# Kernel optimization log

Measured on AMD Instinct MI355X. Metric: run time of the kernel, lower is better.

The kernel has to match this reference:

```python
import jax, jax.numpy as jnp
import numpy as np

B, S, E, H = 1, 2048, 1024, 16
D = E // H  # head_dim = 64
MAX_POS = 2048
NEG_INF = -1e30


def _rotary(x):
    # x: [B, S, H, D]; positions along axis 1
    half = D // 2
    inv_freq = 1.0 / (10000.0 ** (jnp.arange(0, D, 2, dtype=jnp.float32) / D))  # [D/2]
    freqs = jnp.arange(S, dtype=jnp.float32)[:, None] * inv_freq[None, :]       # [S, D/2]
    emb = jnp.concatenate([freqs, freqs], axis=-1)                              # [S, D]
    cos = jnp.cos(emb)[None, :, None, :]
    sin = jnp.sin(emb)[None, :, None, :]
    x1, x2 = x[..., :half], x[..., half:]
    rot = jnp.concatenate([-x2, x1], axis=-1)
    return x * cos + rot * sin


def setup_inputs() -> dict:
    key = jax.random.key(0)
    ks = jax.random.split(key, 8)
    w = lambda k: (jax.random.normal(k, (E, E), jnp.float32) * 0.02)
    inp = {
        "x": jax.random.normal(ks[0], (B, S, E), jnp.float32),
        "mask": jnp.tril(jnp.ones((S, S), jnp.int32)),  # causal 0/1 mask
        "Wq": w(ks[1]), "bq": jnp.zeros((E,), jnp.float32),
        "Wk": w(ks[2]), "bk": jnp.zeros((E,), jnp.float32),
        "Wv": w(ks[3]), "bv": jnp.zeros((E,), jnp.float32),
        "Wo": w(ks[4]), "bo": jnp.zeros((E,), jnp.float32),
        "rel_pos_emb": jax.random.normal(ks[5], (2 * MAX_POS - 1, D), jnp.float32) * 0.02,
    }
    return inp


def reference(x, mask, Wq, bq, Wk, bk, Wv, bv, Wo, bo, rel_pos_emb):
    scale = D ** -0.5
    q = (x @ Wq + bq).reshape(B, S, H, D)
    k = (x @ Wk + bk).reshape(B, S, H, D)
    v = (x @ Wv + bv).reshape(B, S, H, D)
    q = _rotary(q)
    k = _rotary(k)
    # [B, H, S, D]
    qh = jnp.swapaxes(q, 1, 2)
    kh = jnp.swapaxes(k, 1, 2)
    vh = jnp.swapaxes(v, 1, 2)
    scores = jnp.einsum('bhid,bhjd->bhij', qh, kh) * scale  # [B,H,S,S]
    # relative position bias (Shaw-style: gather then contract with q)
    pos = jnp.arange(S)
    bucket = pos[None, :] - pos[:, None] + S - 1            # [S,S] in [0, 2S-2]
    rel = rel_pos_emb[bucket]                               # [S,S,D]
    scores = scores + jnp.einsum('bhid,ijd->bhij', qh, rel)
    scores = jnp.where(mask[None, None, :, :] == 0, NEG_INF, scores)
    attn = jax.nn.softmax(scores, axis=-1)
    out = jnp.einsum('bhij,bhjd->bhid', attn, vh)           # [B,H,S,D]
    out = jnp.swapaxes(out, 1, 2).reshape(B, S, E)
    return out @ Wo + bo
```

## Files before the change

### kernel.cpp

```cpp
#include <hip/hip_runtime.h>
#include <hip/hip_bf16.h>

typedef __attribute__((ext_vector_type(8))) short bf16x8;
typedef __attribute__((ext_vector_type(4))) float f32x4;

#define MFMA16(a,b,c) __builtin_amdgcn_mfma_f32_16x16x32_bf16((a),(b),(c),0,0,0)
#define GLDS16(g, l) __builtin_amdgcn_global_load_lds((const __attribute__((address_space(1))) void*)(g), (__attribute__((address_space(3))) void*)(l), 16, 0, 0)

static constexpr int S_ = 2048, E_ = 1024, H_ = 16;
static constexpr float QS = 0.125f * 1.44269504f;

__device__ __forceinline__ unsigned pk2(float a, float b) {
  __hip_bfloat16 ba = __float2bfloat16(a), bb = __float2bfloat16(b);
  return (unsigned)*(unsigned short*)&ba | ((unsigned)*(unsigned short*)&bb << 16);
}
__device__ __forceinline__ float ubf(unsigned short u) {
  return __uint_as_float((unsigned)u << 16);
}

__global__ __launch_bounds__(256) void prep_k(const float* __restrict__ x, const float* __restrict__ rel,
                                              const float* __restrict__ Wq, const float* __restrict__ Wk,
                                              const float* __restrict__ Wv, const float* __restrict__ Wo,
                                              const float* __restrict__ bq, const float* __restrict__ bk,
                                              const float* __restrict__ bv,
                                              __hip_bfloat16* __restrict__ xb, __hip_bfloat16* __restrict__ relb,
                                              __hip_bfloat16* __restrict__ wqkvT, __hip_bfloat16* __restrict__ woT,
                                              float* __restrict__ bqkv, float* __restrict__ cost,
                                              float* __restrict__ sint) {
  int blk = blockIdx.x, tid = threadIdx.x;
  if (blk < 1024) {
    __shared__ float tile[64][65];
    int wsel = blk >> 8, sub = blk & 255;
    const float* W = wsel == 0 ? Wq : wsel == 1 ? Wk : wsel == 2 ? Wv : Wo;
    __hip_bfloat16* WT = wsel < 3 ? wqkvT + (size_t)wsel * E_ * E_ : woT;
    int bx = sub & 15, by = sub >> 4;
    for (int i = tid; i < 4096; i += 256) {
      int ki = i >> 6, ni = i & 63;
      tile[ki][ni] = W[(size_t)(by*64 + ki) * E_ + bx*64 + ni];
    }
    __syncthreads();
    for (int i = tid; i < 4096; i += 256) {
      int ni = i >> 6, ki = i & 63;
      WT[(size_t)(bx*64 + ni) * E_ + by*64 + ki] = __float2bfloat16(tile[ki][ni]);
    }
  } else if (blk < 3072) {
    int i = (blk - 1024) * 256 + tid;
    float4 v = reinterpret_cast<const float4*>(x)[i];
    xb[4*i+0] = __float2bfloat16(v.x);
    xb[4*i+1] = __float2bfloat16(v.y);
    xb[4*i+2] = __float2bfloat16(v.z);
    xb[4*i+3] = __float2bfloat16(v.w);
  } else if (blk < 3328) {
    int i = (blk - 3072) * 256 + tid;
    if (i < 65520) {
      float4 v = reinterpret_cast<const float4*>(rel)[i];
      relb[4*i+0] = __float2bfloat16(v.x * 8.f);
      relb[4*i+1] = __float2bfloat16(v.y * 8.f);
      relb[4*i+2] = __float2bfloat16(v.z * 8.f);
      relb[4*i+3] = __float2bfloat16(v.w * 8.f);
    }
  } else if (blk < 3584) {
    int idx = (blk - 3328) * 256 + tid;
    int f = idx & 31, s = idx >> 5;
    float inv = powf(10000.f, -(float)f * (1.f/32.f));
    float a = (float)s * inv;
    cost[idx] = cosf(a);
    sint[idx] = sinf(a);
  } else {
    int i = (blk - 3584) * 256 + tid;
    if (i < 3072) bqkv[i] = i < 1024 ? bq[i] : (i < 2048 ? bk[i-1024] : bv[i-2048]);
  }
}

template<int BM, int MODE>
__global__ __launch_bounds__(256) void gemm_k(const __hip_bfloat16* __restrict__ A,
                                              const __hip_bfloat16* __restrict__ BT,
                                              const float* __restrict__ bias,
                                              const float* __restrict__ cost,
                                              const float* __restrict__ sint,
                                              __hip_bfloat16* __restrict__ qhh,
                                              __hip_bfloat16* __restrict__ khh,
                                              __hip_bfloat16* __restrict__ vt,
                                              float* __restrict__ outf,
                                              int K) {
  constexpr int MI = BM/32;
  __shared__ __hip_bfloat16 As[2][BM*64];
  __shared__ __hip_bfloat16 Bs[2][128*64];
  int tid = threadIdx.x, lane = tid & 63, w = tid >> 6;
  int rowq = lane & 15, hi = lane >> 4, ksel = hi << 3;
  int wr = (w >> 1) * (BM/2), wc = (w & 1) * 64;
  int m0 = blockIdx.y * BM, n0 = blockIdx.x * 128;
  int l3 = lane >> 3, l7 = lane & 7;
  f32x4 acc[MI][4] = {};

  auto stage = [&](int k0, int buf) {
    const char* Ap = (const char*)A + ((size_t)(m0 + w*(BM/4)) * K + k0) * 2;
    const char* Bp = (const char*)BT + ((size_t)(n0 + w*32) * K + k0) * 2;
    char* Ad = (char*)&As[buf][w*(BM/4)*64];
    char* Bd = (char*)&Bs[buf][w*32*64];
    for (int i = 0; i < MI; ++i)
      GLDS16(Ap + (size_t)(i*8 + l3)*(K*2) + l7*16, Ad + i*1024);
    for (int i = 0; i < 4; ++i)
      GLDS16(Bp + (size_t)(i*8 + l3)*(K*2) + l7*16, Bd + i*1024);
  };

  stage(0, 0);
  __syncthreads();
  int buf = 0;
  int nk = K >> 6;
  for (int t = 0; t < nk; ++t) {
    if (t + 1 < nk) stage((t+1)*64, buf^1);
    for (int kk = 0; kk < 64; kk += 32) {
      bf16x8 a[MI], b[4];
      for (int i = 0; i < MI; ++i) a[i] = *(const bf16x8*)&As[buf][(wr + i*16 + rowq)*64 + kk + ksel];
      for (int j = 0; j < 4; ++j)  b[j] = *(const bf16x8*)&Bs[buf][(wc + j*16 + rowq)*64 + kk + ksel];
      for (int i = 0; i < MI; ++i)
        for (int j = 0; j < 4; ++j)
          acc[i][j] = MFMA16(a[i], b[j], acc[i][j]);
    }
    __syncthreads();
    buf ^= 1;
  }

  if constexpr (MODE == 0) {
    int matsel = n0 >> 10, ncol = n0 & 1023;
    float bcol[4];
    for (int j = 0; j < 4; ++j) bcol[j] = bias[n0 + wc + j*16 + rowq];
    if (matsel < 2) {
      __hip_bfloat16* dst = matsel ? khh : qhh;
      float qs = matsel ? 1.0f : QS;
      for (int i = 0; i < MI; ++i)
        for (int rg = 0; rg < 4; ++rg) {
          int s = m0 + wr + i*16 + hi*4 + rg;
          for (int j = 0; j < 2; ++j) {
            int colp = ncol + wc + j*16 + rowq;
            int hh = colp >> 6, f = colp & 31;
            float c = cost[s*32 + f], sn = sint[s*32 + f];
            float v1 = acc[i][j][rg]   + bcol[j];
            float v2 = acc[i][j+2][rg] + bcol[j+2];
            dst[((size_t)hh*S_ + s)*64 + f]      = __float2bfloat16((v1*c - v2*sn) * qs);
            dst[((size_t)hh*S_ + s)*64 + f + 32] = __float2bfloat16((v2*c + v1*sn) * qs);
          }
        }
    } else {
      for (int i = 0; i < MI; ++i)
        for (int j = 0; j < 4; ++j) {
          int colp = ncol + wc + j*16 + rowq;
          int hh = colp >> 6, d = colp & 63;
          int s0b = m0 + wr + i*16 + hi*4;
          __hip_bfloat16 tmp[4];
          for (int rg = 0; rg < 4; ++rg)
            tmp[rg] = __float2bfloat16(acc[i][j][rg] + bcol[j]);
          *(ushort4*)(vt + ((size_t)hh*64 + d)*S_ + s0b) = *(ushort4*)tmp;
        }
    }
  } else {
    for (int i = 0; i < MI; ++i)
      for (int rg = 0; rg < 4; ++rg) {
        int row = m0 + wr + i*16 + hi*4 + rg;
        for (int j = 0; j < 4; ++j) {
          int col = n0 + wc + j*16 + rowq;
          outf[(size_t)row*E_ + col] = acc[i][j][rg] + bias[col];
        }
      }
  }
}

__global__ __launch_bounds__(256,2) void attn_k(const __hip_bfloat16* __restrict__ qh,
                                                const __hip_bfloat16* __restrict__ kh,
                                                const __hip_bfloat16* __restrict__ vt,
                                                const __hip_bfloat16* __restrict__ relb,
                                                __hip_bfloat16* __restrict__ opart,
                                                float2* __restrict__ ml) {
  int h = blockIdx.x & 15, p = blockIdx.x >> 4;
  int tid = threadIdx.x, lane = tid & 63, w = tid >> 6;
  int rowq = lane & 15, hi = lane >> 4, ksel = hi << 3;
  int l3 = lane >> 3, l7 = lane & 7;
  int swz = (l7*16) ^ (l3 << 4);
  __shared__ __hip_bfloat16 Ks[2][4096];
  __shared__ __hip_bfloat16 Vs[2][4096];
  __shared__ float Wf[4][16*82];
  __shared__ char  Psb[4][4096];
  float* wrow = &Wf[w][rowq*82];
  char* pp = Psb[w] + rowq*256;
  int sw8 = (rowq & 7) << 4;
  int pcol0 = ((hi*16)      ^ ((rowq & 7) << 4)) >> 1;
  int pcol1 = ((64 + hi*16) ^ ((rowq & 7) << 4)) >> 1;
  int c0 = hi*4 + 15 - rowq;

  for (int ph = 0; ph < 2; ++ph) {
    int qb = ph ? 31 - p : p;
    int T = qb + 1;
    int t0 = ph ? (T + 1) >> 1 : 0;
    int t1 = ph ? T : (T + 1) >> 1;
    int i0w = qb*64 + w*16;

    const __hip_bfloat16* qrow = qh + ((size_t)h*S_ + i0w + rowq)*64 + ksel;
    bf16x8 q0 = *(const bf16x8*)(qrow);
    bf16x8 q1 = *(const bf16x8*)(qrow + 32);
    f32x4 o[4] = {};
    float m = -1e30f, l = 0.f;

    auto stage = [&](int t, int buf) {
      int j0 = t * 64;
      const char* kp = (const char*)(kh + ((size_t)h*S_ + j0 + w*16)*64);
      const char* vp = (const char*)(vt + ((size_t)(h*64 + w*16))*S_ + j0);
      char* kd = (char*)&Ks[buf][w*16*64];
      char* vd = (char*)&Vs[buf][w*16*64];
      for (int i = 0; i < 2; ++i) {
        GLDS16(kp + (size_t)(i*8 + l3)*128  + swz, kd + i*1024);
        GLDS16(vp + (size_t)(i*8 + l3)*4096 + swz, vd + i*1024);
      }
    };
    auto ldrel = [&](int t, bf16x8* rr) {
      const __hip_bfloat16* rp = relb + (size_t)(t*64 - i0w + 2032 + rowq)*64 + ksel;
      #pragma unroll
      for (int nf = 0; nf < 5; ++nf) {
        rr[nf*2]   = *(const bf16x8*)(rp + nf*1024);
        rr[nf*2+1] = *(const bf16x8*)(rp + nf*1024 + 32);
      }
    };

    if (t0 < t1) {
      bf16x8 rc[10];
      ldrel(t0, rc);
      stage(t0, 0);
      __syncthreads();
      int buf = 0;
      for (int t = t0; t < t1; ++t) {
        bool more = (t + 1 < t1);
        if (more) stage(t+1, buf^1);

        f32x4 sa[4] = {};
        f32x4 wt[5] = {};
        __builtin_amdgcn_s_setprio(1);
        for (int kk = 0; kk < 2; ++kk) {
          bf16x8 qf = kk ? q1 : q0;
          int pc = kk ? pcol1 : pcol0;
          for (int nf = 0; nf < 4; ++nf) {
            bf16x8 kf = *(const bf16x8*)&Ks[buf][(nf*16 + rowq)*64 + pc];
            sa[nf] = MFMA16(kf, qf, sa[nf]);
          }
          for (int nf = 0; nf < 5; ++nf)
            wt[nf] = MFMA16(rc[nf*2+kk], qf, wt[nf]);
        }
        __builtin_amdgcn_s_setprio(0);

        #pragma unroll
        for (int nf = 0; nf < 5; ++nf) {
          *(float2*)(wrow + nf*16 + hi*4)     = make_float2(wt[nf][0], wt[nf][1]);
          *(float2*)(wrow + nf*16 + hi*4 + 2) = make_float2(wt[nf][2], wt[nf][3]);
        }

        if (more) ldrel(t+1, rc);

        float sv[4][4];
        #pragma unroll
        for (int rg = 0; rg < 4; ++rg) {
          int cc = c0 + rg;
          #pragma unroll
          for (int nf = 0; nf < 4; ++nf)
            sv[nf][rg] = sa[nf][rg] + wrow[nf*16 + cc];
        }
        float tm = -1e30f;
        bool diag = (t == qb);
        int lim = w*16 + rowq;
        #pragma unroll
        for (int nf = 0; nf < 4; ++nf)
          #pragma unroll
          for (int rg = 0; rg < 4; ++rg) {
            int kl = nf*16 + hi*4 + rg;
            if (diag && kl > lim) sv[nf][rg] = -1e30f;
            tm = fmaxf(tm, sv[nf][rg]);
          }
        tm = fmaxf(tm, __shfl_xor(tm, 16));
        tm = fmaxf(tm, __shfl_xor(tm, 32));

        bool defer = __all(tm <= m + 8.0f);
        float al = 1.0f;
        if (!defer) {
          float mnew = fmaxf(m, tm);
          al = exp2f(m - mnew);
          m = mnew;
        }
        float ls = 0.f;
        float pe[4][4];
        #pragma unroll
        for (int nf = 0; nf < 4; ++nf)
          #pragma unroll
          for (int rg = 0; rg < 4; ++rg) {
            float e = exp2f(sv[nf][rg] - m);
            pe[nf][rg] = e;
            ls += e;
          }
        l = l * al + ls;
        #pragma unroll
        for (int nf = 0; nf < 4; ++nf) {
          uint2 u = { pk2(pe[nf][0], pe[nf][1]), pk2(pe[nf][2], pe[nf][3]) };
          *(uint2*)(pp + ((nf*32 + hi*8) ^ sw8)) = u;
        }
        if (!defer) {
          float alq[4];
          #pragma unroll
          for (int rg = 0; rg < 4; ++rg) alq[rg] = __shfl(al, hi*4 + rg, 16);
          #pragma unroll
          for (int df = 0; df < 4; ++df)
            #pragma unroll
            for (int rg = 0; rg < 4; ++rg) o[df][rg] *= alq[rg];
        }

        __builtin_amdgcn_s_setprio(1);
        for (int kk = 0; kk < 2; ++kk) {
          bf16x8 a = *(const bf16x8*)(pp + ((kk*64 + hi*16) ^ sw8));
          int pc = kk ? pcol1 : pcol0;
          for (int df = 0; df < 4; ++df) {
            bf16x8 b = *(const bf16x8*)&Vs[buf][(df*16 + rowq)*64 + pc];
            o[df] = MFMA16(a, b, o[df]);
          }
        }
        __builtin_amdgcn_s_setprio(0);
        __syncthreads();
        buf ^= 1;
      }
    }

    float lt = l;
    lt += __shfl_xor(lt, 16);
    lt += __shfl_xor(lt, 32);
    if (lane < 16) ml[((size_t)ph*S_ + i0w + rowq)*H_ + h] = make_float2(m, lt);
    #pragma unroll
    for (int df = 0; df < 4; ++df)
      #pragma unroll
      for (int rg = 0; rg < 4; ++rg)
        opart[(size_t)ph*S_*E_ + (size_t)(i0w + hi*4 + rg)*E_ + h*64 + df*16 + rowq] =
            __float2bfloat16(o[df][rg]);
    __syncthreads();
  }
}

__global__ __launch_bounds__(256) void combine_k(const __hip_bfloat16* __restrict__ opart,
                                                 const float2* __restrict__ ml,
                                                 __hip_bfloat16* __restrict__ aout) {
  int r = blockIdx.x, tid = threadIdx.x;
  int c = tid * 4, h = c >> 6;
  float2 a0 = ml[(size_t)r*H_ + h];
  float2 a1 = ml[((size_t)S_ + r)*H_ + h];
  float M = fmaxf(a0.x, a1.x);
  float w0 = exp2f(a0.x - M), w1 = exp2f(a1.x - M);
  float dinv = 1.0f / (w0*a0.y + w1*a1.y);
  w0 *= dinv; w1 *= dinv;
  const unsigned short* o0 = (const unsigned short*)opart + (size_t)r*E_ + c;
  const unsigned short* o1 = o0 + (size_t)S_*E_;
  ushort4 u0 = *(const ushort4*)o0;
  ushort4 u1 = *(const ushort4*)o1;
  __hip_bfloat16 res[4];
  res[0] = __float2bfloat16(w0*ubf(u0.x) + w1*ubf(u1.x));
  res[1] = __float2bfloat16(w0*ubf(u0.y) + w1*ubf(u1.y));
  res[2] = __float2bfloat16(w0*ubf(u0.z) + w1*ubf(u1.z));
  res[3] = __float2bfloat16(w0*ubf(u0.w) + w1*ubf(u1.w));
  *(ushort4*)((unsigned short*)aout + (size_t)r*E_ + c) = *(ushort4*)res;
}

extern "C" void kernel_launch(void* const* d_in, const int* in_sizes, int n_in,
                              void* d_out, int out_size, void* d_ws, size_t ws_size,
                              hipStream_t stream) {
  const float* x   = (const float*)d_in[0];
  const float* Wq  = (const float*)d_in[2];
  const float* bq  = (const float*)d_in[3];
  const float* Wk  = (const float*)d_in[4];
  const float* bk  = (const float*)d_in[5];
  const float* Wv  = (const float*)d_in[6];
  const float* bv  = (const float*)d_in[7];
  const float* Wo  = (const float*)d_in[8];
  const float* bo  = (const float*)d_in[9];
  const float* rel = (const float*)d_in[10];
  float* out = (float*)d_out;

  char* ws = (char*)d_ws;
  size_t off = 0;
  auto alloc = [&](size_t bytes) -> void* {
    void* p = ws + off;
    off = (off + bytes + 255) & ~(size_t)255;
    return p;
  };
  __hip_bfloat16* xb    = (__hip_bfloat16*)alloc((size_t)S_*E_*2);
  __hip_bfloat16* wqkvT = (__hip_bfloat16*)alloc((size_t)3*E_*E_*2);
  float* cost = (float*)alloc((size_t)S_*32*4);
  float* sint = (float*)alloc((size_t)S_*32*4);
  float* bqkv = (float*)alloc((size_t)3072*4);
  if (off < (size_t)16*1024*1024) off = (size_t)16*1024*1024;
  __hip_bfloat16* woT   = (__hip_bfloat16*)alloc((size_t)E_*E_*2);
  __hip_bfloat16* relb  = (__hip_bfloat16*)alloc((size_t)4095*64*2);
  __hip_bfloat16* qhh  = (__hip_bfloat16*)alloc((size_t)S_*E_*2);
  __hip_bfloat16* khh  = (__hip_bfloat16*)alloc((size_t)S_*E_*2);
  __hip_bfloat16* vth  = (__hip_bfloat16*)alloc((size_t)S_*E_*2);
  __hip_bfloat16* aout = (__hip_bfloat16*)alloc((size_t)S_*E_*2);
  float2* ml = (float2*)alloc((size_t)2*S_*H_*8);

  __hip_bfloat16* opart = (__hip_bfloat16*)ws;

  prep_k<<<3596, 256, 0, stream>>>(x, rel, Wq, Wk, Wv, Wo, bq, bk, bv,
                                   xb, relb, wqkvT, woT, bqkv, cost, sint);

  gemm_k<64,0><<<dim3(24,32), 256, 0, stream>>>(xb, wqkvT, bqkv, cost, sint,
                                                qhh, khh, vth, nullptr, E_);

  attn_k<<<512, 256, 0, stream>>>(qhh, khh, vth, relb, opart, ml);
  combine_k<<<S_, 256, 0, stream>>>(opart, ml, aout);

  gemm_k<64,1><<<dim3(8,32), 256, 0, stream>>>(aout, woT, bo, nullptr, nullptr,
                                               nullptr, nullptr, nullptr, out, E_);
}
```

Baseline: 114.4 us.

## Software-pipeline QK and rel-bias MFMAs one tile ahead of softmax

Restructures the attention inner loop so the QK^T and relative-position MFMAs for tile t+1 are issued before the softmax and PV work of tile t. A prologue computes the first tile's scores. K and V loads are staged two tiles ahead, which needs a third V buffer in LDS. The goal is to overlap MFMA work with the softmax VALU and LDS latency. The cost is more registers for the extra score and bias accumulators and about 8KB more LDS per block, which could hurt occupancy.

```diff
diff --git a/kernel.cpp b/kernel.cpp
--- a/kernel.cpp
+++ b/kernel.cpp
@@ -178,7 +178,7 @@
   int l3 = lane >> 3, l7 = lane & 7;
   int swz = (l7*16) ^ (l3 << 4);
   __shared__ __hip_bfloat16 Ks[2][4096];
-  __shared__ __hip_bfloat16 Vs[2][4096];
+  __shared__ __hip_bfloat16 Vs[3][4096];
   __shared__ float Wf[4][16*82];
   __shared__ char  Psb[4][4096];
   float* wrow = &Wf[w][rowq*82];
@@ -201,12 +201,13 @@
     f32x4 o[4] = {};
     float m = -1e30f, l = 0.f;
 
-    auto stage = [&](int t, int buf) {
+    auto stage = [&](int t) {
       int j0 = t * 64;
+      int kb = t & 1, vbuf = t % 3;
       const char* kp = (const char*)(kh + ((size_t)h*S_ + j0 + w*16)*64);
       const char* vp = (const char*)(vt + ((size_t)(h*64 + w*16))*S_ + j0);
-      char* kd = (char*)&Ks[buf][w*16*64];
-      char* vd = (char*)&Vs[buf][w*16*64];
+      char* kd = (char*)&Ks[kb][w*16*64];
+      char* vd = (char*)&Vs[vbuf][w*16*64];
       for (int i = 0; i < 2; ++i) {
         GLDS16(kp + (size_t)(i*8 + l3)*128  + swz, kd + i*1024);
         GLDS16(vp + (size_t)(i*8 + l3)*4096 + swz, vd + i*1024);
@@ -220,39 +221,55 @@
         rr[nf*2+1] = *(const bf16x8*)(rp + nf*1024 + 32);
       }
     };
+    auto qkw = [&](int t, bf16x8* rr, f32x4* sa, f32x4* wt) {
+      int kb = t & 1;
+      __builtin_amdgcn_s_setprio(1);
+      #pragma unroll
+      for (int kk = 0; kk < 2; ++kk) {
+        bf16x8 qf = kk ? q1 : q0;
+        int pc = kk ? pcol1 : pcol0;
+        #pragma unroll
+        for (int nf = 0; nf < 4; ++nf) {
+          bf16x8 kf = *(const bf16x8*)&Ks[kb][(nf*16 + rowq)*64 + pc];
+          sa[nf] = MFMA16(kf, qf, sa[nf]);
+        }
+        #pragma unroll
+        for (int nf = 0; nf < 5; ++nf)
+          wt[nf] = MFMA16(rr[nf*2+kk], qf, wt[nf]);
+      }
+      __builtin_amdgcn_s_setprio(0);
+    };
+    auto wstore = [&](f32x4* wt) {
+      #pragma unroll
+      for (int nf = 0; nf < 5; ++nf) {
+        *(float2*)(wrow + nf*16 + hi*4)     = make_float2(wt[nf][0], wt[nf][1]);
+        *(float2*)(wrow + nf*16 + hi*4 + 2) = make_float2(wt[nf][2], wt[nf][3]);
+      }
+    };
 
     if (t0 < t1) {
       bf16x8 rc[10];
+      stage(t0);
       ldrel(t0, rc);
-      stage(t0, 0);
       __syncthreads();
-      int buf = 0;
+      if (t0 + 1 < t1) stage(t0 + 1);
+      f32x4 saP[4] = {};
+      {
+        f32x4 wtP[5] = {};
+        qkw(t0, rc, saP, wtP);
+        wstore(wtP);
+      }
+      if (t0 + 1 < t1) ldrel(t0 + 1, rc);
+      __syncthreads();
+
       for (int t = t0; t < t1; ++t) {
         bool more = (t + 1 < t1);
-        if (more) stage(t+1, buf^1);
-
-        f32x4 sa[4] = {};
-        f32x4 wt[5] = {};
-        __builtin_amdgcn_s_setprio(1);
-        for (int kk = 0; kk < 2; ++kk) {
-          bf16x8 qf = kk ? q1 : q0;
-          int pc = kk ? pcol1 : pcol0;
-          for (int nf = 0; nf < 4; ++nf) {
-            bf16x8 kf = *(const bf16x8*)&Ks[buf][(nf*16 + rowq)*64 + pc];
-            sa[nf] = MFMA16(kf, qf, sa[nf]);
-          }
-          for (int nf = 0; nf < 5; ++nf)
-            wt[nf] = MFMA16(rc[nf*2+kk], qf, wt[nf]);
-        }
-        __builtin_amdgcn_s_setprio(0);
-
-        #pragma unroll
-        for (int nf = 0; nf < 5; ++nf) {
-          *(float2*)(wrow + nf*16 + hi*4)     = make_float2(wt[nf][0], wt[nf][1]);
-          *(float2*)(wrow + nf*16 + hi*4 + 2) = make_float2(wt[nf][2], wt[nf][3]);
-        }
-
-        if (more) ldrel(t+1, rc);
+        if (t + 2 < t1) stage(t + 2);
+
+        f32x4 saN[4] = {};
+        f32x4 wtN[5] = {};
+        if (more) qkw(t + 1, rc, saN, wtN);
+        if (t + 2 < t1) ldrel(t + 2, rc);
 
         float sv[4][4];
         #pragma unroll
@@ -260,7 +277,7 @@
           int cc = c0 + rg;
           #pragma unroll
           for (int nf = 0; nf < 4; ++nf)
-            sv[nf][rg] = sa[nf][rg] + wrow[nf*16 + cc];
+            sv[nf][rg] = saP[nf][rg] + wrow[nf*16 + cc];
         }
         float tm = -1e30f;
         bool diag = (t == qb);
@@ -309,18 +326,26 @@
             for (int rg = 0; rg < 4; ++rg) o[df][rg] *= alq[rg];
         }
 
+        int vbuf = t % 3;
         __builtin_amdgcn_s_setprio(1);
+        #pragma unroll
         for (int kk = 0; kk < 2; ++kk) {
           bf16x8 a = *(const bf16x8*)(pp + ((kk*64 + hi*16) ^ sw8));
           int pc = kk ? pcol1 : pcol0;
+          #pragma unroll
           for (int df = 0; df < 4; ++df) {
-            bf16x8 b = *(const bf16x8*)&Vs[buf][(df*16 + rowq)*64 + pc];
+            bf16x8 b = *(const bf16x8*)&Vs[vbuf][(df*16 + rowq)*64 + pc];
             o[df] = MFMA16(a, b, o[df]);
           }
         }
         __builtin_amdgcn_s_setprio(0);
+
+        if (more) {
+          wstore(wtN);
+          #pragma unroll
+          for (int nf = 0; nf < 4; ++nf) saP[nf] = saN[nf];
+        }
         __syncthreads();
-        buf ^= 1;
       }
     }
 
```

New measurement: 118.2 us. +3.3%, slower.

## Fuse split-softmax combine into output projection GEMM A-tile staging

Applied to the files above, without the earlier changes.

Removes the separate combine kernel and its intermediate bf16 buffer. The output-projection GEMM gains a new mode that, while staging each A tile, reads both partial attention outputs plus their max and sum statistics, merges them and writes bf16 into shared memory. This saves one kernel launch and a full write and read of the merged activations. In exchange, the A-tile loads become synchronous register loads instead of async global-to-LDS copies, and each of the 8 column blocks recomputes the merge, so partial outputs are read several times.

```diff
diff --git a/kernel.cpp b/kernel.cpp
--- a/kernel.cpp
+++ b/kernel.cpp
@@ -82,6 +82,7 @@
                                               __hip_bfloat16* __restrict__ khh,
                                               __hip_bfloat16* __restrict__ vt,
                                               float* __restrict__ outf,
+                                              const float2* __restrict__ ml2,
                                               int K) {
   constexpr int MI = BM/32;
   __shared__ __hip_bfloat16 As[2][BM*64];
@@ -94,14 +95,42 @@
   f32x4 acc[MI][4] = {};
 
   auto stage = [&](int k0, int buf) {
-    const char* Ap = (const char*)A + ((size_t)(m0 + w*(BM/4)) * K + k0) * 2;
     const char* Bp = (const char*)BT + ((size_t)(n0 + w*32) * K + k0) * 2;
-    char* Ad = (char*)&As[buf][w*(BM/4)*64];
     char* Bd = (char*)&Bs[buf][w*32*64];
-    for (int i = 0; i < MI; ++i)
-      GLDS16(Ap + (size_t)(i*8 + l3)*(K*2) + l7*16, Ad + i*1024);
     for (int i = 0; i < 4; ++i)
       GLDS16(Bp + (size_t)(i*8 + l3)*(K*2) + l7*16, Bd + i*1024);
+    if constexpr (MODE != 2) {
+      const char* Ap = (const char*)A + ((size_t)(m0 + w*(BM/4)) * K + k0) * 2;
+      char* Ad = (char*)&As[buf][w*(BM/4)*64];
+      for (int i = 0; i < MI; ++i)
+        GLDS16(Ap + (size_t)(i*8 + l3)*(K*2) + l7*16, Ad + i*1024);
+    } else {
+      int hh = k0 >> 6;
+      #pragma unroll
+      for (int i = 0; i < MI; ++i) {
+        int row = m0 + w*(BM/4) + i*8 + l3;
+        const int* o0 = (const int*)((const unsigned short*)A + (size_t)row*E_ + k0 + l7*8);
+        int4 u0 = *(const int4*)o0;
+        int4 u1 = *(const int4*)(o0 + (size_t)S_*E_/2);
+        float2 a0 = ml2[(size_t)row*H_ + hh];
+        float2 a1 = ml2[((size_t)S_ + row)*H_ + hh];
+        float M = fmaxf(a0.x, a1.x);
+        float w0 = exp2f(a0.x - M), w1 = exp2f(a1.x - M);
+        float dinv = 1.0f / (w0*a0.y + w1*a1.y);
+        w0 *= dinv; w1 *= dinv;
+        auto comb2 = [&](int x0, int x1) -> unsigned {
+          float lo = w0*ubf((unsigned short)(x0 & 0xffff)) + w1*ubf((unsigned short)(x1 & 0xffff));
+          float hiv = w0*ubf((unsigned short)((unsigned)x0 >> 16)) + w1*ubf((unsigned short)((unsigned)x1 >> 16));
+          return pk2(lo, hiv);
+        };
+        int res[4];
+        res[0] = (int)comb2(u0.x, u1.x);
+        res[1] = (int)comb2(u0.y, u1.y);
+        res[2] = (int)comb2(u0.z, u1.z);
+        res[3] = (int)comb2(u0.w, u1.w);
+        *(int4*)&As[buf][(w*(BM/4) + i*8 + l3)*64 + l7*8] = *(int4*)res;
+      }
+    }
   };
 
   stage(0, 0);
@@ -338,29 +367,6 @@
   }
 }
 
-__global__ __launch_bounds__(256) void combine_k(const __hip_bfloat16* __restrict__ opart,
-                                                 const float2* __restrict__ ml,
-                                                 __hip_bfloat16* __restrict__ aout) {
-  int r = blockIdx.x, tid = threadIdx.x;
-  int c = tid * 4, h = c >> 6;
-  float2 a0 = ml[(size_t)r*H_ + h];
-  float2 a1 = ml[((size_t)S_ + r)*H_ + h];
-  float M = fmaxf(a0.x, a1.x);
-  float w0 = exp2f(a0.x - M), w1 = exp2f(a1.x - M);
-  float dinv = 1.0f / (w0*a0.y + w1*a1.y);
-  w0 *= dinv; w1 *= dinv;
-  const unsigned short* o0 = (const unsigned short*)opart + (size_t)r*E_ + c;
-  const unsigned short* o1 = o0 + (size_t)S_*E_;
-  ushort4 u0 = *(const ushort4*)o0;
-  ushort4 u1 = *(const ushort4*)o1;
-  __hip_bfloat16 res[4];
-  res[0] = __float2bfloat16(w0*ubf(u0.x) + w1*ubf(u1.x));
-  res[1] = __float2bfloat16(w0*ubf(u0.y) + w1*ubf(u1.y));
-  res[2] = __float2bfloat16(w0*ubf(u0.z) + w1*ubf(u1.z));
-  res[3] = __float2bfloat16(w0*ubf(u0.w) + w1*ubf(u1.w));
-  *(ushort4*)((unsigned short*)aout + (size_t)r*E_ + c) = *(ushort4*)res;
-}
-
 extern "C" void kernel_launch(void* const* d_in, const int* in_sizes, int n_in,
                               void* d_out, int out_size, void* d_ws, size_t ws_size,
                               hipStream_t stream) {
@@ -394,7 +400,6 @@
   __hip_bfloat16* qhh  = (__hip_bfloat16*)alloc((size_t)S_*E_*2);
   __hip_bfloat16* khh  = (__hip_bfloat16*)alloc((size_t)S_*E_*2);
   __hip_bfloat16* vth  = (__hip_bfloat16*)alloc((size_t)S_*E_*2);
-  __hip_bfloat16* aout = (__hip_bfloat16*)alloc((size_t)S_*E_*2);
   float2* ml = (float2*)alloc((size_t)2*S_*H_*8);
 
   __hip_bfloat16* opart = (__hip_bfloat16*)ws;
@@ -403,11 +408,10 @@
                                    xb, relb, wqkvT, woT, bqkv, cost, sint);
 
   gemm_k<64,0><<<dim3(24,32), 256, 0, stream>>>(xb, wqkvT, bqkv, cost, sint,
-                                                qhh, khh, vth, nullptr, E_);
+                                                qhh, khh, vth, nullptr, nullptr, E_);
 
   attn_k<<<512, 256, 0, stream>>>(qhh, khh, vth, relb, opart, ml);
-  combine_k<<<S_, 256, 0, stream>>>(opart, ml, aout);
-
-  gemm_k<64,1><<<dim3(8,32), 256, 0, stream>>>(aout, woT, bo, nullptr, nullptr,
-                                               nullptr, nullptr, nullptr, out, E_);
-}
+
+  gemm_k<64,2><<<dim3(8,32), 256, 0, stream>>>(opart, woT, bo, nullptr, nullptr,
+                                               nullptr, nullptr, nullptr, out, ml, E_);
+}
```

New measurement: 120.5 us. 1.05x slower.
